# Kernel optimization log

Measured on AMD Instinct MI355X. Metric: run time of the kernel, lower is better.

Reference implementation:

```python
import jax, jax.numpy as jnp
import numpy as np

H, W_DIM, D = 16, 16, 16
RADIUS = 5
O_I = 10.0
O_X = 4.0


def setup_inputs() -> dict:
    key = jax.random.key(0)
    k1, k2 = jax.random.split(key)
    labels = jax.random.uniform(k1, (2, 4, H, W_DIM, D), dtype=jnp.float32)
    inputs = jax.random.uniform(k2, (2, 1, H, W_DIM, D), dtype=jnp.float32)
    return {"labels": labels, "inputs": inputs}


def _spatial_weights():
    # Pairwise squared spatial distances between flattened voxels in (H,W,D)
    # row-major order -- matches the torch swapaxes/flatten sequence.
    ii, jj, kk = jnp.meshgrid(jnp.arange(H), jnp.arange(W_DIM), jnp.arange(D), indexing='ij')
    coords = jnp.stack([ii, jj, kk], axis=-1).reshape(-1, 3)  # (P, 3)
    diffs = coords[:, None, :] - coords[None, :, :]           # (P, P, 3)
    sqd = jnp.sum(diffs * diffs, axis=-1).astype(jnp.float32)  # (P, P)
    mask = (sqd <= float(RADIUS ** 2)).astype(jnp.float32)
    W_X = jnp.exp(-sqd / O_X) * mask
    return mask, W_X


def reference(labels, inputs):
    N, C = inputs.shape[0], inputs.shape[1]
    K = labels.shape[1]
    P = H * W_DIM * D
    mask, W_X = _spatial_weights()

    # get_weights: intensity affinity, masked, times spatial affinity
    flat = inputs.reshape(N, C, P)
    I_diff = flat[:, :, :, None] - flat[:, :, None, :]        # (N,C,P,P)
    masked_I_diff = I_diff * mask                              # matches torch mul-before-square
    W_I = jnp.exp(-(masked_I_diff ** 2) / O_I) * mask
    Wm = W_I * W_X                                             # (N,C,P,P)

    A = labels.reshape(N, K, P)                                # (N,K,P)
    # numerator_k[n,c] = sum_pq A[n,k,p] A[n,k,q] W[n,c,p,q]
    num = jnp.einsum('nkp,ncpq,nkq->nkc', A, Wm, A)
    # denominator_k[n,c] = sum_pq A[n,k,q] W[n,c,p,q]
    den = jnp.einsum('ncpq,nkq->nkc', Wm, A)
    loss = jnp.sum(num / (den + 1e-8), axis=(1, 2))            # (N,)
    return jnp.float32(K) - loss
```

## Files before the change

kernel.cpp:

```cpp
#include <hip/hip_runtime.h>

namespace {
constexpr int P        = 4096;
constexpr int KC       = 4;
constexpr int NS       = 81;
constexpr int BLOCK    = 256;
constexpr int PER_N    = NS * P;
constexpr int BLK_N    = PER_N / BLOCK;
constexpr int NBLK     = 2 * BLK_N;

struct Tab {
    signed char di[NS], dj[NS], ir[NS], sq2[NS];
};
constexpr Tab make_tab() {
    Tab t{};
    int idx = 0;
    for (int a = -5; a <= 5; ++a)
        for (int b = -5; b <= 5; ++b) {
            int s2 = a * a + b * b;
            if (s2 <= 25) {
                t.di[idx] = (signed char)a;
                t.dj[idx] = (signed char)b;
                int rem = 25 - s2, r = 0;
                while ((r + 1) * (r + 1) <= rem) ++r;
                t.ir[idx]  = (signed char)r;
                t.sq2[idx] = (signed char)s2;
                ++idx;
            }
        }
    return t;
}
}

__device__ constexpr Tab TAB = make_tab();

__global__ __launch_bounds__(BLOCK) void sncut_main(
        const float* __restrict__ labels,
        const float* __restrict__ inputs,
        float* __restrict__ partials) {
    const int b     = blockIdx.x;
    const int n     = (b >= BLK_N) ? 1 : 0;
    const int local = (b - n * BLK_N) * BLOCK + threadIdx.x;
    const int s     = local >> 12;
    const int p     = local & (P - 1);

    const int di  = TAB.di[s];
    const int dj  = TAB.dj[s];
    const int ir  = TAB.ir[s];
    const int sq2 = TAB.sq2[s];

    const int i  = p >> 8;
    const int j  = (p >> 4) & 15;
    const int kz = p & 15;
    const int ii = i + di;
    const int jj = j + dj;

    const float* __restrict__ inp = inputs + n * P;
    const float* __restrict__ A   = labels + n * KC * P;

    float s_w = 0.f, s_k0 = 0.f, s_k1 = 0.f, s_k2 = 0.f, s_k3 = 0.f;

    if ((unsigned)ii < 16u && (unsigned)jj < 16u) {
        const float Ip   = inp[p];
        const int   base = p + di * 256 + dj * 16;
        const int   lo   = (-kz > -ir) ? -kz : -ir;
        const int   hi   = (15 - kz < ir) ? (15 - kz) : ir;
        for (int dk = lo; dk <= hi; ++dk) {
            const int   q = base + dk;
            const float d = Ip - inp[q];
            const float w = __expf(-0.25f * (float)(sq2 + dk * dk) - 0.1f * d * d);
            s_w  += w;
            s_k0 += w * A[q];
            s_k1 += w * A[P + q];
            s_k2 += w * A[2 * P + q];
            s_k3 += w * A[3 * P + q];
        }
    }

    float vals[8];
    {
        const float a0 = A[p];
        const float a1 = A[P + p];
        const float a2 = A[2 * P + p];
        const float a3 = A[3 * P + p];
        vals[0] = a0 * s_k0;
        vals[1] = a1 * s_k1;
        vals[2] = a2 * s_k2;
        vals[3] = a3 * s_k3;
        vals[4] = a0 * s_w;
        vals[5] = a1 * s_w;
        vals[6] = a2 * s_w;
        vals[7] = a3 * s_w;
    }

    #pragma unroll
    for (int off = 32; off >= 1; off >>= 1) {
        #pragma unroll
        for (int t = 0; t < 8; ++t)
            vals[t] += __shfl_down(vals[t], off, 64);
    }

    __shared__ float red[4][8];
    const int lane = threadIdx.x & 63;
    const int wid  = threadIdx.x >> 6;
    if (lane == 0) {
        #pragma unroll
        for (int t = 0; t < 8; ++t) red[wid][t] = vals[t];
    }
    __syncthreads();
    if (threadIdx.x < 8) {
        partials[b * 8 + threadIdx.x] =
            red[0][threadIdx.x] + red[1][threadIdx.x] +
            red[2][threadIdx.x] + red[3][threadIdx.x];
    }
}

__global__ __launch_bounds__(256) void finalize_k(
        const float* __restrict__ partials, float* __restrict__ out) {
    __shared__ float sm[2][256];
    const int t  = threadIdx.x;
    const int c  = t & 7;
    const int g2 = t >> 3;
    float a0 = 0.f, a1 = 0.f;
    for (int b = g2; b < NBLK; b += 32) {
        const float v = partials[b * 8 + c];
        if (b < BLK_N) a0 += v; else a1 += v;
    }
    sm[0][t] = a0;
    sm[1][t] = a1;
    __syncthreads();
    if (t < 16) {
        const int n = t >> 3, cc = t & 7;
        float sacc = 0.f;
        for (int k = 0; k < 32; ++k) sacc += sm[n][cc + 8 * k];
        sm[n][cc] = sacc;
    }
    __syncthreads();
    if (t < 2) {
        float loss = 0.f;
        #pragma unroll
        for (int k = 0; k < 4; ++k)
            loss += sm[t][k] / (sm[t][4 + k] + 1e-8f);
        out[t] = (float)KC - loss;
    }
}

extern "C" void kernel_launch(void* const* d_in, const int* in_sizes, int n_in,
                              void* d_out, int out_size, void* d_ws, size_t ws_size,
                              hipStream_t stream) {
    const float* labels = (const float*)d_in[0];
    const float* inputs = (const float*)d_in[1];
    float* partials = (float*)d_ws;
    float* out      = (float*)d_out;

    hipLaunchKernelGGL(sncut_main, dim3(NBLK), dim3(BLOCK), 0, stream,
                       labels, inputs, partials);
    hipLaunchKernelGGL(finalize_k, dim3(1), dim3(256), 0, stream,
                       partials, out);
}
```

Before: 82.93 us.

## Fuse finalize into main kernel with last-block reduction and 3 stencil rows per thread

```diff
diff --git a/kernel.cpp b/kernel.cpp
--- a/kernel.cpp
+++ b/kernel.cpp
@@ -1,13 +1,14 @@
 #include <hip/hip_runtime.h>
 
 namespace {
-constexpr int P        = 4096;
-constexpr int KC       = 4;
-constexpr int NS       = 81;
-constexpr int BLOCK    = 256;
-constexpr int PER_N    = NS * P;
-constexpr int BLK_N    = PER_N / BLOCK;
-constexpr int NBLK     = 2 * BLK_N;
+constexpr int P     = 4096;
+constexpr int KC    = 4;
+constexpr int NS    = 81;
+constexpr int NGRP  = 27;
+constexpr int BLOCK = 256;
+constexpr int PBLK  = P / BLOCK;
+constexpr int BLK_N = NGRP * PBLK;
+constexpr int NBLK  = 2 * BLK_N;
 
 struct Tab {
     signed char di[NS], dj[NS], ir[NS], sq2[NS];
@@ -34,46 +35,57 @@
 
 __device__ constexpr Tab TAB = make_tab();
 
-__global__ __launch_bounds__(BLOCK) void sncut_main(
+__device__ float g_partials[NBLK * 8];
+__device__ int   g_count = 0;
+
+__global__ __launch_bounds__(BLOCK) void sncut_fused(
         const float* __restrict__ labels,
         const float* __restrict__ inputs,
-        float* __restrict__ partials) {
-    const int b     = blockIdx.x;
-    const int n     = (b >= BLK_N) ? 1 : 0;
-    const int local = (b - n * BLK_N) * BLOCK + threadIdx.x;
-    const int s     = local >> 12;
-    const int p     = local & (P - 1);
-
-    const int di  = TAB.di[s];
-    const int dj  = TAB.dj[s];
-    const int ir  = TAB.ir[s];
-    const int sq2 = TAB.sq2[s];
+        float* __restrict__ out) {
+    const int b  = blockIdx.x;
+    const int n  = (b >= BLK_N) ? 1 : 0;
+    const int lb = b - n * BLK_N;
+    const int g  = lb >> 4;
+    const int pb = lb & 15;
+    const int p  = pb * BLOCK + threadIdx.x;
 
     const int i  = p >> 8;
     const int j  = (p >> 4) & 15;
     const int kz = p & 15;
-    const int ii = i + di;
-    const int jj = j + dj;
 
     const float* __restrict__ inp = inputs + n * P;
     const float* __restrict__ A   = labels + n * KC * P;
 
+    const float Ip = inp[p];
+
     float s_w = 0.f, s_k0 = 0.f, s_k1 = 0.f, s_k2 = 0.f, s_k3 = 0.f;
 
-    if ((unsigned)ii < 16u && (unsigned)jj < 16u) {
-        const float Ip   = inp[p];
-        const int   base = p + di * 256 + dj * 16;
-        const int   lo   = (-kz > -ir) ? -kz : -ir;
-        const int   hi   = (15 - kz < ir) ? (15 - kz) : ir;
-        for (int dk = lo; dk <= hi; ++dk) {
-            const int   q = base + dk;
-            const float d = Ip - inp[q];
-            const float w = __expf(-0.25f * (float)(sq2 + dk * dk) - 0.1f * d * d);
-            s_w  += w;
-            s_k0 += w * A[q];
-            s_k1 += w * A[P + q];
-            s_k2 += w * A[2 * P + q];
-            s_k3 += w * A[3 * P + q];
+    #pragma unroll
+    for (int sub = 0; sub < 3; ++sub) {
+        const int s   = g + NGRP * sub;
+        const int di  = TAB.di[s];
+        const int dj  = TAB.dj[s];
+        const int ir  = TAB.ir[s];
+        const int sq2 = TAB.sq2[s];
+
+        const int ii = i + di;
+        const int jj = j + dj;
+
+        if ((unsigned)ii < 16u && (unsigned)jj < 16u) {
+            const int base = p + di * 256 + dj * 16;
+            const int lo   = (-kz > -ir) ? -kz : -ir;
+            const int hi   = (15 - kz < ir) ? (15 - kz) : ir;
+            for (int dk = lo; dk <= hi; ++dk) {
+                const int   q = base + dk;
+                const float d = Ip - inp[q];
+                const float w = __expf(-0.25f * (float)(sq2 + dk * dk)
+                                       - 0.1f * d * d);
+                s_w  += w;
+                s_k0 += w * A[q];
+                s_k1 += w * A[P + q];
+                s_k2 += w * A[2 * P + q];
+                s_k3 += w * A[3 * P + q];
+            }
         }
     }
 
@@ -101,6 +113,7 @@
     }
 
     __shared__ float red[4][8];
+    __shared__ bool  is_last;
     const int lane = threadIdx.x & 63;
     const int wid  = threadIdx.x >> 6;
     if (lane == 0) {
@@ -108,40 +121,46 @@
         for (int t = 0; t < 8; ++t) red[wid][t] = vals[t];
     }
     __syncthreads();
-    if (threadIdx.x < 8) {
-        partials[b * 8 + threadIdx.x] =
-            red[0][threadIdx.x] + red[1][threadIdx.x] +
-            red[2][threadIdx.x] + red[3][threadIdx.x];
-    }
-}
 
-__global__ __launch_bounds__(256) void finalize_k(
-        const float* __restrict__ partials, float* __restrict__ out) {
-    __shared__ float sm[2][256];
-    const int t  = threadIdx.x;
-    const int c  = t & 7;
-    const int g2 = t >> 3;
-    float a0 = 0.f, a1 = 0.f;
-    for (int b = g2; b < NBLK; b += 32) {
-        const float v = partials[b * 8 + c];
-        if (b < BLK_N) a0 += v; else a1 += v;
-    }
-    sm[0][t] = a0;
-    sm[1][t] = a1;
-    __syncthreads();
-    if (t < 16) {
-        const int n = t >> 3, cc = t & 7;
-        float sacc = 0.f;
-        for (int k = 0; k < 32; ++k) sacc += sm[n][cc + 8 * k];
-        sm[n][cc] = sacc;
+    if (threadIdx.x == 0) {
+        #pragma unroll
+        for (int t = 0; t < 8; ++t)
+            g_partials[b * 8 + t] =
+                red[0][t] + red[1][t] + red[2][t] + red[3][t];
+        __threadfence();
+        is_last = (atomicAdd(&g_count, 1) == NBLK - 1);
     }
     __syncthreads();
-    if (t < 2) {
-        float loss = 0.f;
-        #pragma unroll
-        for (int k = 0; k < 4; ++k)
-            loss += sm[t][k] / (sm[t][4 + k] + 1e-8f);
-        out[t] = (float)KC - loss;
+
+    if (is_last) {
+        __threadfence();
+        __shared__ float sm[2][256];
+        const int t  = threadIdx.x;
+        const int c  = t & 7;
+        const int g2 = t >> 3;
+        float a0 = 0.f, a1 = 0.f;
+        for (int bb = g2; bb < NBLK; bb += 32) {
+            const float v = g_partials[bb * 8 + c];
+            if (bb < BLK_N) a0 += v; else a1 += v;
+        }
+        sm[0][t] = a0;
+        sm[1][t] = a1;
+        __syncthreads();
+        if (t < 16) {
+            const int nn = t >> 3, cc = t & 7;
+            float sacc = 0.f;
+            for (int k = 0; k < 32; ++k) sacc += sm[nn][cc + 8 * k];
+            sm[nn][cc] = sacc;
+        }
+        __syncthreads();
+        if (t < 2) {
+            float loss = 0.f;
+            #pragma unroll
+            for (int k = 0; k < 4; ++k)
+                loss += sm[t][k] / (sm[t][4 + k] + 1e-8f);
+            out[t] = (float)KC - loss;
+        }
+        if (t == 0) atomicExch(&g_count, 0);
     }
 }
 
@@ -150,11 +169,9 @@
                               hipStream_t stream) {
     const float* labels = (const float*)d_in[0];
     const float* inputs = (const float*)d_in[1];
-    float* partials = (float*)d_ws;
-    float* out      = (float*)d_out;
+    float* out = (float*)d_out;
+    (void)d_ws; (void)ws_size;
 
-    hipLaunchKernelGGL(sncut_main, dim3(NBLK), dim3(BLOCK), 0, stream,
-                       labels, inputs, partials);
-    hipLaunchKernelGGL(finalize_k, dim3(1), dim3(256), 0, stream,
-                       partials, out);
+    hipLaunchKernelGGL(sncut_fused, dim3(NBLK), dim3(BLOCK), 0, stream,
+                       labels, inputs, out);
 }
```

Measured after the change: 83.35 us. About the same (+0.5%).
